# Optimization experiments

Hardware: AMD Instinct MI355X
Metric: run time of the kernel (lower is better)

The kernel has to match this reference:

```python
import jax, jax.numpy as jnp
import numpy as np

B, D, H, W = 64, 64, 32, 32
K = 1024


def setup_inputs() -> dict:
    key = jax.random.key(0)
    k1, k2 = jax.random.split(key)
    latents = jax.random.normal(k1, (B, D, H, W), dtype=jnp.float32)
    # nn.Embedding(K, D) initialized uniform(-1/K, 1/K)
    embedding = jax.random.uniform(k2, (K, D), dtype=jnp.float32,
                                   minval=-1.0 / K, maxval=1.0 / K)
    return {"latents": latents, "embedding": embedding}


def reference(latents, embedding):
    # [B, D, H, W] -> [B, H, W, D]
    x = jnp.transpose(latents, (0, 2, 3, 1))
    x_shape = x.shape
    flat = x.reshape(-1, x_shape[-1])  # [N, D], N = B*H*W
    # squared euclidean distances to each code: [N, K]
    dist = (jnp.sum(flat ** 2, axis=1, keepdims=True)
            + jnp.sum(embedding ** 2, axis=1)
            - 2.0 * flat @ embedding.T)
    encoding_inds = jnp.argmin(dist, axis=1)  # [N]
    # gather codes (equivalent to one_hot @ embedding)
    quantized = embedding[encoding_inds].reshape(x_shape)  # [B, H, W, D]
    commitment_loss = jnp.mean((jax.lax.stop_gradient(quantized) - x) ** 2)
    embedding_loss = jnp.mean((quantized - jax.lax.stop_gradient(x)) ** 2)
    # straight-through estimator
    quantized_st = x + jax.lax.stop_gradient(quantized - x)
    q_out = jnp.transpose(quantized_st, (0, 3, 1, 2))  # [B, D, H, W]
    return q_out, commitment_loss, embedding_loss, encoding_inds
```

## Files before the change

kernel.cpp:

```cpp
#include <hip/hip_runtime.h>

#define QSIZE 4194304
#define WS_E2_OFF   0
#define WS_ET_OFF   4096

__global__ void k0_prep(const float* __restrict__ emb, float* __restrict__ embT,
                        float* __restrict__ e2, float* __restrict__ out) {
    #pragma clang fp contract(off)
    if (blockIdx.x < 256) {
        int g = blockIdx.x * 256 + threadIdx.x;
        int d = g >> 10, k = g & 1023;
        embT[g] = emb[k * 64 + d];
    } else {
        #pragma unroll 1
        for (int j = 0; j < 4; ++j) {
            int k = j * 256 + threadIdx.x;
            const float* e = emb + k * 64;
            float r[8];
            #pragma unroll
            for (int q = 0; q < 8; ++q) r[q] = e[q] * e[q];
            #pragma unroll
            for (int i = 8; i < 64; i += 8) {
                #pragma unroll
                for (int q = 0; q < 8; ++q) r[q] = r[q] + e[i + q] * e[i + q];
            }
            e2[k] = ((r[0] + r[1]) + (r[2] + r[3])) + ((r[4] + r[5]) + (r[6] + r[7]));
        }
        if (threadIdx.x < 2) out[QSIZE + threadIdx.x] = 0.f;
    }
}

__launch_bounds__(512, 8)
__global__ void k1_argmin(const float* __restrict__ lat, const float* __restrict__ embT,
                          const float* __restrict__ e2t, const float* __restrict__ emb,
                          float* __restrict__ out) {
    #pragma clang fp contract(off)
    __shared__ float2 xs2[32][64];
    __shared__ float sm1[8][64];
    __shared__ int   sbi[8][64];
    __shared__ int   sbiF[64];
    __shared__ float red[8];

    const int tid  = threadIdx.x;
    const int lane = tid & 63;
    const int w    = tid >> 6;
    const int row0 = blockIdx.x * 64;
    const int row  = row0 + lane;
    const int b    = row >> 10;
    const int hw   = row & 1023;

    {
        const float* latb = lat + (size_t)b * 65536 + (row0 & 1023);
        #pragma unroll
        for (int i = 0; i < 8; ++i) {
            const int idx = i * 512 + tid;
            const int d = idx >> 6, r = idx & 63;
            ((float*)&xs2[d >> 1][r])[d & 1] = latb[d * 1024 + r];
        }
    }
    __syncthreads();

    float x2;
    {
        float r[8];
        #pragma unroll
        for (int j = 0; j < 8; ++j) {
            const float v = ((const float*)&xs2[j >> 1][lane])[j & 1];
            r[j] = v * v;
        }
        #pragma unroll
        for (int i = 8; i < 64; i += 8) {
            #pragma unroll
            for (int j = 0; j < 8; ++j) {
                const float v = ((const float*)&xs2[(i + j) >> 1][lane])[(i + j) & 1];
                r[j] = r[j] + v * v;
            }
        }
        x2 = ((r[0] + r[1]) + (r[2] + r[3])) + ((r[4] + r[5]) + (r[6] + r[7]));
    }

    const int kbase = __builtin_amdgcn_readfirstlane(w) << 7;
    float m1 = 3.4e38f;
    int   bi = kbase;
    #pragma unroll 1
    for (int g = 0; g < 8; ++g) {
        const int k0 = kbase + (g << 4);
        const float* __restrict__ ed  = embT + k0;
        const float* __restrict__ e2g = e2t + k0;
        float c[16];
        #pragma unroll
        for (int j = 0; j < 16; ++j) c[j] = 0.f;
        #pragma unroll 2
        for (int dd = 0; dd < 32; ++dd) {
            const float2 xv = xs2[dd][lane];
            const float* e0 = ed + (dd << 11);
            #pragma unroll
            for (int j = 0; j < 16; ++j) c[j] = __builtin_fmaf(xv.x, e0[j], c[j]);
            const float* e1 = e0 + 1024;
            #pragma unroll
            for (int j = 0; j < 16; ++j) c[j] = __builtin_fmaf(xv.y, e1[j], c[j]);
        }
        #pragma unroll
        for (int j = 0; j < 16; ++j) {
            const float t  = x2 + e2g[j];
            const float dv = t - 2.0f * c[j];
            if (dv < m1) { m1 = dv; bi = k0 + j; }
        }
    }
    sm1[w][lane] = m1;
    sbi[w][lane] = bi;
    __syncthreads();

    if (w == 0) {
        float M1 = sm1[0][lane];
        int   BI = sbi[0][lane];
        #pragma unroll
        for (int ww = 1; ww < 8; ++ww) {
            const float a = sm1[ww][lane];
            if (a < M1) { M1 = a; BI = sbi[ww][lane]; }
        }
        sbiF[lane] = BI;
        out[QSIZE + 2 + row] = (float)BI;
    }
    __syncthreads();

    {
        const float* xg = lat + (size_t)b * 65536 + hw;
        const int BI = sbiF[lane];
        const float* er = emb + BI * 64 + w * 8;
        float sq = 0.f;
        #pragma unroll
        for (int j4 = 0; j4 < 2; ++j4) {
            const float4 q4 = *(const float4*)(er + j4 * 4);
            #pragma unroll
            for (int j2 = 0; j2 < 4; ++j2) {
                const int d = w * 8 + j4 * 4 + j2;
                const float xv  = xg[d * 1024];
                const float qv  = (&q4.x)[j2];
                const float qmx = qv - xv;
                out[(size_t)b * 65536 + d * 1024 + hw] = xv + qmx;
                sq = __builtin_fmaf(qmx, qmx, sq);
            }
        }
        #pragma unroll
        for (int off = 32; off > 0; off >>= 1) sq += __shfl_down(sq, off, 64);
        if (lane == 0) red[w] = sq;
    }
    __syncthreads();
    if (tid == 0) {
        const float p = (((red[0] + red[1]) + (red[2] + red[3]))
                       + ((red[4] + red[5]) + (red[6] + red[7]))) * (1.0f / 4194304.0f);
        atomicAdd(&out[QSIZE],     p);
        atomicAdd(&out[QSIZE + 1], p);
    }
}

extern "C" void kernel_launch(void* const* d_in, const int* in_sizes, int n_in,
                              void* d_out, int out_size, void* d_ws, size_t ws_size,
                              hipStream_t stream) {
    const float* lat = (const float*)d_in[0];
    const float* emb = (const float*)d_in[1];
    float* out  = (float*)d_out;
    char*  ws   = (char*)d_ws;
    float* e2t  = (float*)(ws + WS_E2_OFF);
    float* embT = (float*)(ws + WS_ET_OFF);

    hipLaunchKernelGGL(k0_prep,   dim3(257),  dim3(256), 0, stream, emb, embT, e2t, out);
    hipLaunchKernelGGL(k1_argmin, dim3(1024), dim3(512), 0, stream, lat, embT, e2t, emb, out);
}
```

Baseline: 183.6 us.

## Use split-bf16 MFMA distance search with fp32 rescue of near-tie rows

Replaces the fp32 FMA distance loop with bf16 MFMA matrix ops that split latents and codebook into high and low bf16 parts (three products) to approximate fp32 dot products. The kernel tracks the best and second-best distance per row, and rows whose margin falls below a fixed threshold go onto a list. A rescue kernel recomputes those rows exactly in fp32, and a separate elementwise kernel writes the quantized output, indices and losses. The aim is to move the dominant compute onto matrix cores. In exchange it adds two extra launches and atomics, and exact argmin agreement depends on the fixed threshold.

Measured after the change: 335.9 us. +82.9%, slower.

```diff
diff --git a/kernel.cpp b/kernel.cpp
--- a/kernel.cpp
+++ b/kernel.cpp
@@ -1,155 +1,312 @@
 #include <hip/hip_runtime.h>
 
 #define QSIZE 4194304
-#define WS_E2_OFF   0
-#define WS_ET_OFF   4096
-
-__global__ void k0_prep(const float* __restrict__ emb, float* __restrict__ embT,
-                        float* __restrict__ e2, float* __restrict__ out) {
+#define THR   1.5e-4f
+
+#define WS_E2   0
+#define WS_EH   4096
+#define WS_EL   135168
+#define WS_IND  266240
+#define WS_CNT  397312
+#define WS_LIST 397328
+
+typedef __attribute__((ext_vector_type(8))) short short8;
+typedef __attribute__((ext_vector_type(4))) float f32x4;
+
+__device__ inline ushort bf16_rne(float v) {
+    union { float f; unsigned u; } a; a.f = v;
+    return (ushort)((a.u + 0x7FFFu + ((a.u >> 16) & 1u)) >> 16);
+}
+__device__ inline float bf16_f(ushort h) {
+    union { unsigned u; float f; } a; a.u = ((unsigned)h) << 16;
+    return a.f;
+}
+
+__global__ void k0_prep(const float* __restrict__ emb, float* __restrict__ e2,
+                        ushort* __restrict__ eh, ushort* __restrict__ el,
+                        unsigned* __restrict__ cnt, float* __restrict__ out) {
     #pragma clang fp contract(off)
-    if (blockIdx.x < 256) {
-        int g = blockIdx.x * 256 + threadIdx.x;
-        int d = g >> 10, k = g & 1023;
-        embT[g] = emb[k * 64 + d];
-    } else {
-        #pragma unroll 1
+    int k = blockIdx.x * 256 + threadIdx.x;
+    const float* e = emb + k * 64;
+    float r[8];
+    #pragma unroll
+    for (int q = 0; q < 8; ++q) r[q] = e[q] * e[q];
+    #pragma unroll
+    for (int i = 8; i < 64; i += 8) {
+        #pragma unroll
+        for (int q = 0; q < 8; ++q) r[q] = r[q] + e[i + q] * e[i + q];
+    }
+    e2[k] = ((r[0] + r[1]) + (r[2] + r[3])) + ((r[4] + r[5]) + (r[6] + r[7]));
+    #pragma unroll 4
+    for (int d = 0; d < 64; ++d) {
+        float v = e[d];
+        ushort h = bf16_rne(v);
+        eh[k * 64 + d] = h;
+        el[k * 64 + d] = bf16_rne(v - bf16_f(h));
+    }
+    if (k == 0) { *cnt = 0u; out[QSIZE] = 0.f; out[QSIZE + 1] = 0.f; }
+}
+
+__launch_bounds__(256, 2)
+__global__ void k1_mfma(const float* __restrict__ lat, const ushort* __restrict__ eh,
+                        const ushort* __restrict__ el, const float* __restrict__ e2,
+                        ushort* __restrict__ ind, unsigned* __restrict__ cnt,
+                        ushort* __restrict__ list) {
+    #pragma clang fp contract(off)
+    __shared__ ushort xls[2][128][64];
+
+    const int tid  = threadIdx.x;
+    const int lane = tid & 63;
+    const int w    = tid >> 6;
+    const int lm   = lane & 15;
+    const int lg   = lane >> 4;
+    const int br   = blockIdx.x;
+    const int b    = br >> 3;
+    const int hw0  = (br & 7) * 128;
+
+    {
+        const float* latb = lat + (size_t)b * 65536 + hw0;
+        #pragma unroll 4
+        for (int i = 0; i < 32; ++i) {
+            int idx = i * 256 + tid;
+            int d = idx >> 7, r = idx & 127;
+            float v = latb[d * 1024 + r];
+            ushort h = bf16_rne(v);
+            ushort l2 = bf16_rne(v - bf16_f(h));
+            int dsw = d ^ ((r & 7) << 3);
+            xls[0][r][dsw] = h;
+            xls[1][r][dsw] = l2;
+        }
+    }
+    __syncthreads();
+
+    short8 ah[2][2], al[2][2];
+    #pragma unroll
+    for (int rt = 0; rt < 2; ++rt) {
+        int r = w * 32 + rt * 16 + lm;
+        #pragma unroll
+        for (int kh = 0; kh < 2; ++kh) {
+            int d0 = (lg * 8 + kh * 32) ^ ((r & 7) << 3);
+            ah[rt][kh] = *(const short8*)&xls[0][r][d0];
+            al[rt][kh] = *(const short8*)&xls[1][r][d0];
+        }
+    }
+
+    const ushort* ehp = eh + lm * 64 + lg * 8;
+    const ushort* elp = el + lm * 64 + lg * 8;
+    float m1[2][4], m2[2][4];
+    int   bi[2][4];
+    #pragma unroll
+    for (int rt = 0; rt < 2; ++rt)
+        #pragma unroll
+        for (int j = 0; j < 4; ++j) { m1[rt][j] = 3.4e38f; m2[rt][j] = 3.4e38f; bi[rt][j] = 0; }
+
+    const f32x4 zero4 = {0.f, 0.f, 0.f, 0.f};
+    short8 cbh0 = *(const short8*)(ehp);
+    short8 cbh1 = *(const short8*)(ehp + 32);
+    short8 cbl0 = *(const short8*)(elp);
+    short8 cbl1 = *(const short8*)(elp + 32);
+    float  ce2  = e2[lm];
+
+    #pragma unroll 1
+    for (int ct = 0; ct < 64; ++ct) {
+        const int cto = (ct < 63 ? ct + 1 : 63) * 1024;
+        short8 nbh0 = *(const short8*)(ehp + cto);
+        short8 nbh1 = *(const short8*)(ehp + cto + 32);
+        short8 nbl0 = *(const short8*)(elp + cto);
+        short8 nbl1 = *(const short8*)(elp + cto + 32);
+        float  ne2  = e2[(ct < 63 ? ct + 1 : 63) * 16 + lm];
+
+        f32x4 acc0, acc1;
+        acc0 = __builtin_amdgcn_mfma_f32_16x16x32_bf16(ah[0][0], cbh0, zero4, 0, 0, 0);
+        acc1 = __builtin_amdgcn_mfma_f32_16x16x32_bf16(ah[1][0], cbh0, zero4, 0, 0, 0);
+        acc0 = __builtin_amdgcn_mfma_f32_16x16x32_bf16(ah[0][1], cbh1, acc0, 0, 0, 0);
+        acc1 = __builtin_amdgcn_mfma_f32_16x16x32_bf16(ah[1][1], cbh1, acc1, 0, 0, 0);
+        acc0 = __builtin_amdgcn_mfma_f32_16x16x32_bf16(ah[0][0], cbl0, acc0, 0, 0, 0);
+        acc1 = __builtin_amdgcn_mfma_f32_16x16x32_bf16(ah[1][0], cbl0, acc1, 0, 0, 0);
+        acc0 = __builtin_amdgcn_mfma_f32_16x16x32_bf16(ah[0][1], cbl1, acc0, 0, 0, 0);
+        acc1 = __builtin_amdgcn_mfma_f32_16x16x32_bf16(ah[1][1], cbl1, acc1, 0, 0, 0);
+        acc0 = __builtin_amdgcn_mfma_f32_16x16x32_bf16(al[0][0], cbh0, acc0, 0, 0, 0);
+        acc1 = __builtin_amdgcn_mfma_f32_16x16x32_bf16(al[1][0], cbh0, acc1, 0, 0, 0);
+        acc0 = __builtin_amdgcn_mfma_f32_16x16x32_bf16(al[0][1], cbh1, acc0, 0, 0, 0);
+        acc1 = __builtin_amdgcn_mfma_f32_16x16x32_bf16(al[1][1], cbh1, acc1, 0, 0, 0);
+
+        const int code = ct * 16 + lm;
+        #pragma unroll
         for (int j = 0; j < 4; ++j) {
-            int k = j * 256 + threadIdx.x;
-            const float* e = emb + k * 64;
+            {
+                float dv = __builtin_fmaf(-2.f, acc0[j], ce2);
+                bool lt = dv < m1[0][j];
+                m2[0][j] = lt ? m1[0][j] : fminf(m2[0][j], dv);
+                bi[0][j] = lt ? code : bi[0][j];
+                m1[0][j] = lt ? dv : m1[0][j];
+            }
+            {
+                float dv = __builtin_fmaf(-2.f, acc1[j], ce2);
+                bool lt = dv < m1[1][j];
+                m2[1][j] = lt ? m1[1][j] : fminf(m2[1][j], dv);
+                bi[1][j] = lt ? code : bi[1][j];
+                m1[1][j] = lt ? dv : m1[1][j];
+            }
+        }
+        cbh0 = nbh0; cbh1 = nbh1; cbl0 = nbl0; cbl1 = nbl1; ce2 = ne2;
+    }
+
+    #pragma unroll
+    for (int rt = 0; rt < 2; ++rt) {
+        #pragma unroll
+        for (int j = 0; j < 4; ++j) {
+            float M1 = m1[rt][j], M2 = m2[rt][j];
+            int   I1 = bi[rt][j];
+            #pragma unroll
+            for (int m = 1; m <= 8; m <<= 1) {
+                float om1 = __shfl_xor(M1, m, 64);
+                float om2 = __shfl_xor(M2, m, 64);
+                int   oi1 = __shfl_xor(I1, m, 64);
+                bool take = (om1 < M1) || (om1 == M1 && oi1 < I1);
+                float loser = take ? M1 : om1;
+                M2 = fminf(fminf(M2, om2), loser);
+                M1 = take ? om1 : M1;
+                I1 = take ? oi1 : I1;
+            }
+            if (lm == 0) {
+                int grow = br * 128 + w * 32 + rt * 16 + lg * 4 + j;
+                if (M2 - M1 > THR) {
+                    ind[grow] = (ushort)I1;
+                } else {
+                    unsigned p = atomicAdd(cnt, 1u);
+                    list[p] = (ushort)grow;
+                }
+            }
+        }
+    }
+}
+
+__launch_bounds__(512, 8)
+__global__ void k2_rescue(const float* __restrict__ lat, const float* __restrict__ emb,
+                          const float* __restrict__ e2, const unsigned* __restrict__ cnt,
+                          const ushort* __restrict__ list, ushort* __restrict__ ind) {
+    #pragma clang fp contract(off)
+    __shared__ float2 xs2[32][64];
+    __shared__ float  sm1[8][64];
+    __shared__ int    sbi[8][64];
+    __shared__ int    rl[64];
+
+    const int tid  = threadIdx.x;
+    const int lane = tid & 63;
+    const int w    = tid >> 6;
+    const unsigned n = *cnt;
+
+    for (unsigned base = blockIdx.x * 64u; base < n; base += gridDim.x * 64u) {
+        if (tid < 64) {
+            unsigned idx = base + tid;
+            rl[tid] = (int)list[idx < n ? idx : base];
+        }
+        __syncthreads();
+
+        const int rowL = rl[lane];
+        const float* xg = lat + (size_t)(rowL >> 10) * 65536 + (rowL & 1023);
+        #pragma unroll
+        for (int i = 0; i < 8; ++i) {
+            int d = i * 8 + w;
+            ((float*)&xs2[d >> 1][lane])[d & 1] = xg[d * 1024];
+        }
+        __syncthreads();
+
+        float x2;
+        {
             float r[8];
             #pragma unroll
-            for (int q = 0; q < 8; ++q) r[q] = e[q] * e[q];
+            for (int j = 0; j < 8; ++j) {
+                const float v = ((const float*)&xs2[j >> 1][lane])[j & 1];
+                r[j] = v * v;
+            }
             #pragma unroll
             for (int i = 8; i < 64; i += 8) {
                 #pragma unroll
-                for (int q = 0; q < 8; ++q) r[q] = r[q] + e[i + q] * e[i + q];
-            }
-            e2[k] = ((r[0] + r[1]) + (r[2] + r[3])) + ((r[4] + r[5]) + (r[6] + r[7]));
-        }
-        if (threadIdx.x < 2) out[QSIZE + threadIdx.x] = 0.f;
-    }
-}
-
-__launch_bounds__(512, 8)
-__global__ void k1_argmin(const float* __restrict__ lat, const float* __restrict__ embT,
-                          const float* __restrict__ e2t, const float* __restrict__ emb,
-                          float* __restrict__ out) {
+                for (int j = 0; j < 8; ++j) {
+                    const float v = ((const float*)&xs2[(i + j) >> 1][lane])[(i + j) & 1];
+                    r[j] = r[j] + v * v;
+                }
+            }
+            x2 = ((r[0] + r[1]) + (r[2] + r[3])) + ((r[4] + r[5]) + (r[6] + r[7]));
+        }
+
+        const int kbase = __builtin_amdgcn_readfirstlane(w) << 7;
+        float m1v = 3.4e38f;
+        int   biv = kbase;
+        #pragma unroll 1
+        for (int kk = 0; kk < 128; kk += 4) {
+            const float* ep = emb + (size_t)(kbase + kk) * 64;
+            float c0 = 0.f, c1 = 0.f, c2 = 0.f, c3 = 0.f;
+            #pragma unroll 2
+            for (int dd = 0; dd < 32; ++dd) {
+                const float2 xv = xs2[dd][lane];
+                c0 = __builtin_fmaf(xv.x, ep[2*dd],       c0);
+                c0 = __builtin_fmaf(xv.y, ep[2*dd + 1],   c0);
+                c1 = __builtin_fmaf(xv.x, ep[64 + 2*dd],  c1);
+                c1 = __builtin_fmaf(xv.y, ep[64 + 2*dd+1],c1);
+                c2 = __builtin_fmaf(xv.x, ep[128 + 2*dd], c2);
+                c2 = __builtin_fmaf(xv.y, ep[128+2*dd+1], c2);
+                c3 = __builtin_fmaf(xv.x, ep[192 + 2*dd], c3);
+                c3 = __builtin_fmaf(xv.y, ep[192+2*dd+1], c3);
+            }
+            const float e20 = e2[kbase + kk + 0];
+            const float e21 = e2[kbase + kk + 1];
+            const float e22 = e2[kbase + kk + 2];
+            const float e23 = e2[kbase + kk + 3];
+            const float t0 = x2 + e20; const float d0v = t0 - 2.0f * c0;
+            const float t1 = x2 + e21; const float d1v = t1 - 2.0f * c1;
+            const float t2 = x2 + e22; const float d2v = t2 - 2.0f * c2;
+            const float t3 = x2 + e23; const float d3v = t3 - 2.0f * c3;
+            if (d0v < m1v) { m1v = d0v; biv = kbase + kk + 0; }
+            if (d1v < m1v) { m1v = d1v; biv = kbase + kk + 1; }
+            if (d2v < m1v) { m1v = d2v; biv = kbase + kk + 2; }
+            if (d3v < m1v) { m1v = d3v; biv = kbase + kk + 3; }
+        }
+        sm1[w][lane] = m1v;
+        sbi[w][lane] = biv;
+        __syncthreads();
+        if (w == 0) {
+            float M1 = sm1[0][lane];
+            int   BI = sbi[0][lane];
+            #pragma unroll
+            for (int ww = 1; ww < 8; ++ww) {
+                const float a = sm1[ww][lane];
+                if (a < M1) { M1 = a; BI = sbi[ww][lane]; }
+            }
+            ind[rowL] = (ushort)BI;
+        }
+        __syncthreads();
+    }
+}
+
+__launch_bounds__(256)
+__global__ void k3_qout(const float* __restrict__ lat, const float* __restrict__ emb,
+                        const ushort* __restrict__ ind, float* __restrict__ out) {
     #pragma clang fp contract(off)
-    __shared__ float2 xs2[32][64];
-    __shared__ float sm1[8][64];
-    __shared__ int   sbi[8][64];
-    __shared__ int   sbiF[64];
-    __shared__ float red[8];
-
-    const int tid  = threadIdx.x;
-    const int lane = tid & 63;
-    const int w    = tid >> 6;
-    const int row0 = blockIdx.x * 64;
-    const int row  = row0 + lane;
-    const int b    = row >> 10;
-    const int hw   = row & 1023;
-
-    {
-        const float* latb = lat + (size_t)b * 65536 + (row0 & 1023);
-        #pragma unroll
-        for (int i = 0; i < 8; ++i) {
-            const int idx = i * 512 + tid;
-            const int d = idx >> 6, r = idx & 63;
-            ((float*)&xs2[d >> 1][r])[d & 1] = latb[d * 1024 + r];
-        }
-    }
+    __shared__ float red[4];
+    const int t = threadIdx.x;
+    float sq = 0.f;
+    #pragma unroll
+    for (int i = 0; i < 8; ++i) {
+        int g  = blockIdx.x * 2048 + i * 256 + t;
+        int bb = g >> 16, d = (g >> 10) & 63, hw = g & 1023;
+        int nidx = (bb << 10) + hw;
+        int id = (int)ind[nidx];
+        float q  = emb[id * 64 + d];
+        float xv = lat[g];
+        float qmx = q - xv;
+        out[g] = xv + qmx;
+        sq = __builtin_fmaf(qmx, qmx, sq);
+        if (d == 0) out[QSIZE + 2 + nidx] = (float)id;
+    }
+    #pragma unroll
+    for (int off = 32; off > 0; off >>= 1) sq += __shfl_down(sq, off, 64);
+    if ((t & 63) == 0) red[t >> 6] = sq;
     __syncthreads();
-
-    float x2;
-    {
-        float r[8];
-        #pragma unroll
-        for (int j = 0; j < 8; ++j) {
-            const float v = ((const float*)&xs2[j >> 1][lane])[j & 1];
-            r[j] = v * v;
-        }
-        #pragma unroll
-        for (int i = 8; i < 64; i += 8) {
-            #pragma unroll
-            for (int j = 0; j < 8; ++j) {
-                const float v = ((const float*)&xs2[(i + j) >> 1][lane])[(i + j) & 1];
-                r[j] = r[j] + v * v;
-            }
-        }
-        x2 = ((r[0] + r[1]) + (r[2] + r[3])) + ((r[4] + r[5]) + (r[6] + r[7]));
-    }
-
-    const int kbase = __builtin_amdgcn_readfirstlane(w) << 7;
-    float m1 = 3.4e38f;
-    int   bi = kbase;
-    #pragma unroll 1
-    for (int g = 0; g < 8; ++g) {
-        const int k0 = kbase + (g << 4);
-        const float* __restrict__ ed  = embT + k0;
-        const float* __restrict__ e2g = e2t + k0;
-        float c[16];
-        #pragma unroll
-        for (int j = 0; j < 16; ++j) c[j] = 0.f;
-        #pragma unroll 2
-        for (int dd = 0; dd < 32; ++dd) {
-            const float2 xv = xs2[dd][lane];
-            const float* e0 = ed + (dd << 11);
-            #pragma unroll
-            for (int j = 0; j < 16; ++j) c[j] = __builtin_fmaf(xv.x, e0[j], c[j]);
-            const float* e1 = e0 + 1024;
-            #pragma unroll
-            for (int j = 0; j < 16; ++j) c[j] = __builtin_fmaf(xv.y, e1[j], c[j]);
-        }
-        #pragma unroll
-        for (int j = 0; j < 16; ++j) {
-            const float t  = x2 + e2g[j];
-            const float dv = t - 2.0f * c[j];
-            if (dv < m1) { m1 = dv; bi = k0 + j; }
-        }
-    }
-    sm1[w][lane] = m1;
-    sbi[w][lane] = bi;
-    __syncthreads();
-
-    if (w == 0) {
-        float M1 = sm1[0][lane];
-        int   BI = sbi[0][lane];
-        #pragma unroll
-        for (int ww = 1; ww < 8; ++ww) {
-            const float a = sm1[ww][lane];
-            if (a < M1) { M1 = a; BI = sbi[ww][lane]; }
-        }
-        sbiF[lane] = BI;
-        out[QSIZE + 2 + row] = (float)BI;
-    }
-    __syncthreads();
-
-    {
-        const float* xg = lat + (size_t)b * 65536 + hw;
-        const int BI = sbiF[lane];
-        const float* er = emb + BI * 64 + w * 8;
-        float sq = 0.f;
-        #pragma unroll
-        for (int j4 = 0; j4 < 2; ++j4) {
-            const float4 q4 = *(const float4*)(er + j4 * 4);
-            #pragma unroll
-            for (int j2 = 0; j2 < 4; ++j2) {
-                const int d = w * 8 + j4 * 4 + j2;
-                const float xv  = xg[d * 1024];
-                const float qv  = (&q4.x)[j2];
-                const float qmx = qv - xv;
-                out[(size_t)b * 65536 + d * 1024 + hw] = xv + qmx;
-                sq = __builtin_fmaf(qmx, qmx, sq);
-            }
-        }
-        #pragma unroll
-        for (int off = 32; off > 0; off >>= 1) sq += __shfl_down(sq, off, 64);
-        if (lane == 0) red[w] = sq;
-    }
-    __syncthreads();
-    if (tid == 0) {
-        const float p = (((red[0] + red[1]) + (red[2] + red[3]))
-                       + ((red[4] + red[5]) + (red[6] + red[7]))) * (1.0f / 4194304.0f);
+    if (t == 0) {
+        float p = ((red[0] + red[1]) + (red[2] + red[3])) * (1.0f / 4194304.0f);
         atomicAdd(&out[QSIZE],     p);
         atomicAdd(&out[QSIZE + 1], p);
     }
@@ -160,11 +317,17 @@
                               hipStream_t stream) {
     const float* lat = (const float*)d_in[0];
     const float* emb = (const float*)d_in[1];
-    float* out  = (float*)d_out;
-    char*  ws   = (char*)d_ws;
-    float* e2t  = (float*)(ws + WS_E2_OFF);
-    float* embT = (float*)(ws + WS_ET_OFF);
-
-    hipLaunchKernelGGL(k0_prep,   dim3(257),  dim3(256), 0, stream, emb, embT, e2t, out);
-    hipLaunchKernelGGL(k1_argmin, dim3(1024), dim3(512), 0, stream, lat, embT, e2t, emb, out);
-}
+    float* out = (float*)d_out;
+    char*  ws  = (char*)d_ws;
+    float*    e2   = (float*)(ws + WS_E2);
+    ushort*   eh   = (ushort*)(ws + WS_EH);
+    ushort*   el   = (ushort*)(ws + WS_EL);
+    ushort*   ind  = (ushort*)(ws + WS_IND);
+    unsigned* cnt  = (unsigned*)(ws + WS_CNT);
+    ushort*   list = (ushort*)(ws + WS_LIST);
+
+    hipLaunchKernelGGL(k0_prep,   dim3(4),    dim3(256), 0, stream, emb, e2, eh, el, cnt, out);
+    hipLaunchKernelGGL(k1_mfma,   dim3(512),  dim3(256), 0, stream, lat, eh, el, e2, ind, cnt, list);
+    hipLaunchKernelGGL(k2_rescue, dim3(64),   dim3(512), 0, stream, lat, emb, e2, cnt, list, ind);
+    hipLaunchKernelGGL(k3_qout,   dim3(2048), dim3(256), 0, stream, lat, emb, ind, out);
+}
```
